# Optimization experiments

Measured on AMD Instinct MI355X. Metric: run time of the kernel, lower is better.

The kernel has to match this reference:

```python
import jax, jax.numpy as jnp
import numpy as np
from jax import lax

D, B, C, H, HD, FF, NC = 6, 32, 384, 6, 64, 1536, 10
IMG, P = 224, 16
N = (IMG // P) ** 2 + 1  # 197 tokens incl cls
SCALE = HD ** -0.5
EPS = 1e-6


def ln(x, w, b):
    m = jnp.mean(x, axis=-1, keepdims=True)
    v = jnp.var(x, axis=-1, keepdims=True)
    return (x - m) * lax.rsqrt(v + EPS) * w + b


def setup_inputs() -> dict:
    key = jax.random.key(0)
    ks = iter(jax.random.split(key, 40))
    rn = lambda shape, s=0.02: jax.random.normal(next(ks), shape, jnp.float32) * s
    inp = {
        'x': jax.random.normal(next(ks), (B, 3, IMG, IMG), jnp.float32),
        'y': jax.random.randint(next(ks), (B,), 0, NC),
        'patch_w': rn((C, 3, P, P)),
        'patch_b': rn((C,)),
        'cls_token': rn((1, 1, C)),
        'pos_embed': rn((1, N, C)),
        'n1_w': jnp.ones((D, C)), 'n1_b': jnp.zeros((D, C)),
        'qkv_w': rn((D, 3 * C, C)), 'qkv_b': rn((D, 3 * C)),
        'proj_w': rn((D, C, C)), 'proj_b': rn((D, C)),
        'mask_attn': jnp.ones((D, NC, H, HD)) + rn((D, NC, H, HD), 0.01),
        'mask_proj': jnp.ones((D, NC, C, C)) + rn((D, NC, C, C), 0.01),
        'n2_w': jnp.ones((D, C)), 'n2_b': jnp.zeros((D, C)),
        'fc1_w': rn((D, FF, C)), 'fc1_b': rn((D, FF)),
        'fc2_w': rn((D, C, FF)), 'fc2_b': rn((D, C)),
        'mask_fc1': jnp.ones((D, NC, FF, C)) + rn((D, NC, FF, C), 0.01),
        'mask_fc2': jnp.ones((D, NC, C, FF)) + rn((D, NC, C, FF), 0.01),
        'norm_w': jnp.ones((C,)), 'norm_b': jnp.zeros((C,)),
        'head_w': rn((NC, C)), 'head_b': jnp.zeros((NC,)),
    }
    return inp


def reference(x, y, patch_w, patch_b, cls_token, pos_embed, n1_w, n1_b, qkv_w,
              qkv_b, proj_w, proj_b, mask_attn, mask_proj, n2_w, n2_b,
              fc1_w, fc1_b, fc2_w, fc2_b, mask_fc1, mask_fc2,
              norm_w, norm_b, head_w, head_b):
    # patch embed: conv P x P stride P -> (B, C, 14, 14) -> (B, 196, C)
    h = lax.conv_general_dilated(x, patch_w, (P, P), 'VALID',
                                 dimension_numbers=('NCHW', 'OIHW', 'NCHW'))
    h = h.reshape(B, C, -1).transpose(0, 2, 1) + patch_b
    h = jnp.concatenate([jnp.broadcast_to(cls_token, (B, 1, C)), h], axis=1)
    h = h + pos_embed

    def block(xc, p):
        (w1n, b1n, qw, qb, pw, pb, ma, mp, w2n, b2n,
         f1w, f1b, f2w, f2b, mf1, mf2) = p
        t = ln(xc, w1n, b1n)
        qkv = (t @ qw.T + qb).reshape(B, N, 3, H, HD).transpose(2, 0, 3, 1, 4)
        q, k, v = qkv[0], qkv[1], qkv[2]  # (B,H,N,HD)
        a = jax.nn.softmax((q * SCALE) @ k.transpose(0, 1, 3, 2), axis=-1)
        o = a @ v  # (B,H,N,HD)
        o = o * ma[y][:, :, None, :]  # per-class head/dim mask
        o = o.transpose(0, 2, 1, 3).reshape(B, N, C)
        Wp = pw[None] * mp[y]  # (B,C,C) per-sample masked proj
        attn_out = jnp.einsum('bni,boi->bno', o, Wp) + pb
        xc = xc + attn_out
        t = ln(xc, w2n, b2n)
        W1 = f1w[None] * mf1[y]  # (B,FF,C)
        t = jnp.einsum('bni,boi->bno', t, W1) + f1b
        t = jax.nn.gelu(t, approximate=False)
        W2 = f2w[None] * mf2[y]  # (B,C,FF)
        t = jnp.einsum('bni,boi->bno', t, W2) + f2b
        return xc + t, None

    xs = (n1_w, n1_b, qkv_w, qkv_b, proj_w, proj_b, mask_attn, mask_proj,
          n2_w, n2_b, fc1_w, fc1_b, fc2_w, fc2_b, mask_fc1, mask_fc2)
    h, _ = lax.scan(block, h, xs)
    h = ln(h, norm_w, norm_b)
    cls = h[:, 0]  # (B, C)
    return cls @ head_w.T + head_b
```

## Files before the change

kernel.cpp:

```cpp
#include <hip/hip_runtime.h>
#include <hip/hip_bf16.h>
#include <math.h>

#define Dn 6
#define Bn 32
#define Cn 384
#define Hn 6
#define HDn 64
#define FFn 1536
#define NCn 10
#define IMGn 224
#define Nn 197
#define NPATCH 196
#define RP 256
#define TROWS 6400
#define SCALEf 0.125f
#define EPSf 1e-6f

typedef unsigned short u16;
typedef __attribute__((ext_vector_type(8))) short short8;
typedef __attribute__((ext_vector_type(4))) float f32x4;

__device__ __forceinline__ u16 f2bf(float f) {
    unsigned u = __float_as_uint(f);
    return (u16)((u + 0x7FFFu + ((u >> 16) & 1u)) >> 16);
}

__device__ __forceinline__ void gload16(const void* g, void* l) {
    __builtin_amdgcn_global_load_lds((const __attribute__((address_space(1))) void*)g,
                                     (__attribute__((address_space(3))) void*)l, 16, 0, 0);
}

__global__ __launch_bounds__(256) void cvtbf_kernel(const float* __restrict__ in,
                                                    u16* __restrict__ out) {
    long off = ((long)blockIdx.x * 256 + threadIdx.x) * 8;
    float4 v0 = *(const float4*)(in + off);
    float4 v1 = *(const float4*)(in + off + 4);
    short8 p;
    p[0] = f2bf(v0.x); p[1] = f2bf(v0.y); p[2] = f2bf(v0.z); p[3] = f2bf(v0.w);
    p[4] = f2bf(v1.x); p[5] = f2bf(v1.y); p[6] = f2bf(v1.z); p[7] = f2bf(v1.w);
    *(short8*)(out + off) = p;
}

__global__ __launch_bounds__(256) void maskmul3_kernel(
    const float* __restrict__ pw, const float* __restrict__ mp,
    const float* __restrict__ f1w, const float* __restrict__ mf1,
    const float* __restrict__ f2w, const float* __restrict__ mf2,
    u16* __restrict__ WMp, u16* __restrict__ WMf1, u16* __restrict__ WMf2) {
    const int seg = blockIdx.y;
    const unsigned bx = blockIdx.x;
    const float* W; const float* M; u16* O; int wi;
    if (seg == 0) {
        if (bx >= 720u) return;
        unsigned cls = bx / 72u;
        wi = (int)(bx - cls * 72u) * 2048 + threadIdx.x * 8;
        W = pw;
        M = mp + (long)cls * (Cn * Cn);
        O = WMp + (long)cls * (Cn * Cn);
    } else if (seg == 1) {
        unsigned cls = bx / 288u;
        wi = (int)(bx - cls * 288u) * 2048 + threadIdx.x * 8;
        W = f1w;
        M = mf1 + (long)cls * (FFn * Cn);
        O = WMf1 + (long)cls * (FFn * Cn);
    } else {
        unsigned cls = bx / 288u;
        wi = (int)(bx - cls * 288u) * 2048 + threadIdx.x * 8;
        W = f2w;
        M = mf2 + (long)cls * (Cn * FFn);
        O = WMf2 + (long)cls * (Cn * FFn);
    }
    float4 w0 = *(const float4*)(W + wi);
    float4 w1 = *(const float4*)(W + wi + 4);
    float4 m0 = *(const float4*)(M + wi);
    float4 m1 = *(const float4*)(M + wi + 4);
    short8 p;
    p[0] = f2bf(w0.x * m0.x); p[1] = f2bf(w0.y * m0.y);
    p[2] = f2bf(w0.z * m0.z); p[3] = f2bf(w0.w * m0.w);
    p[4] = f2bf(w1.x * m1.x); p[5] = f2bf(w1.y * m1.y);
    p[6] = f2bf(w1.z * m1.z); p[7] = f2bf(w1.w * m1.w);
    *(short8*)(O + wi) = p;
}

__global__ __launch_bounds__(256) void im2col_kernel(const float* __restrict__ x,
                                                     u16* __restrict__ col) {
    long idx = (long)blockIdx.x * 256 + threadIdx.x;
    int k = (int)(idx % 768);
    long row = idx / 768;
    int b = (int)(row / NPATCH), p = (int)(row % NPATCH);
    int i = k / 256, r = k % 256, ph = r / 16, pw = r % 16;
    int py = p / 14, px = p % 14;
    col[idx] = f2bf(x[(((long)b * 3 + i) * IMGn + py * 16 + ph) * IMGn + px * 16 + pw]);
}

__global__ __launch_bounds__(256) void assemble_kernel(const float* __restrict__ tmp,
                                                       const float* __restrict__ cls_token,
                                                       const float* __restrict__ pos,
                                                       float* __restrict__ x) {
    long idx = (long)blockIdx.x * 256 + threadIdx.x;
    int c = (int)(idx % Cn);
    long rem = idx / Cn;
    int n = (int)(rem % Nn);
    int b = (int)(rem / Nn);
    float v;
    if (n == 0) v = cls_token[c];
    else v = tmp[((long)b * NPATCH + (n - 1)) * Cn + c];
    x[((long)b * RP + n) * Cn + c] = v + pos[n * Cn + c];
}

__global__ __launch_bounds__(256) void pad_zero(float* __restrict__ X,
                                                u16* __restrict__ Tp) {
    int b = blockIdx.x;
    int tid = threadIdx.x;
    if (b == Bn) {
        u16* t0 = Tp + (long)Bn * Nn * Cn;
        for (int i = tid; i < (TROWS - Bn * Nn) * Cn; i += 256) t0[i] = 0;
        return;
    }
    float* Xb = X + ((long)b * RP + Nn) * Cn;
    for (int i = tid; i < (RP - Nn) * Cn; i += 256) Xb[i] = 0.f;
}

__global__ __launch_bounds__(64) void ln_kernel(const float* __restrict__ x,
                                                const float* __restrict__ w,
                                                const float* __restrict__ b,
                                                u16* __restrict__ out) {
    long blk = blockIdx.x;
    int bb = (int)(blk / Nn), n = (int)(blk % Nn);
    const float* xr = x + ((long)bb * RP + n) * Cn;
    u16* orow = out + ((long)bb * Nn + n) * Cn;
    int lane = threadIdx.x;
    float v[6];
    float s = 0.f, ss = 0.f;
#pragma unroll
    for (int j = 0; j < 6; ++j) {
        v[j] = xr[lane + 64 * j];
        s += v[j];
        ss += v[j] * v[j];
    }
#pragma unroll
    for (int off = 32; off >= 1; off >>= 1) {
        s += __shfl_xor(s, off);
        ss += __shfl_xor(ss, off);
    }
    float m = s * (1.0f / Cn);
    float var = ss * (1.0f / Cn) - m * m;
    float rstd = rsqrtf(var + EPSf);
#pragma unroll
    for (int j = 0; j < 6; ++j) {
        int c = lane + 64 * j;
        orow[c] = f2bf((v[j] - m) * rstd * w[c] + b[c]);
    }
}

template <int EPI, int MT>
__global__ __launch_bounds__(256) void gemm_bf16(
    const u16* __restrict__ A, long strideA,
    const u16* __restrict__ Wb, long wClassStride,
    const int* __restrict__ y,
    const float* __restrict__ bias,
    void* __restrict__ OutV, long strideO,
    int Nout, int Ktot) {
    const int bz = blockIdx.z;
    A += (long)bz * strideA;
    const u16* Wp = Wb + (y ? (long)y[bz] * wClassStride : 0);

    constexpr int ASUB = MT / 16;
    constexpr int AI = MT / 32;
    __shared__ alignas(16) u16 Ab[2][ASUB * 512];
    __shared__ alignas(16) u16 Bb[2][4096];

    const int tid = threadIdx.x;
    const int lane = tid & 63;
    const int w = tid >> 6;
    const int wr = w >> 1, wc = w & 1;
    const int m0 = blockIdx.x * MT;
    const int n0 = blockIdx.y * 128;
    const int r15 = lane & 15, oct = lane >> 4;

    auto STAGE = [&](int k0, int bf) {
        {
            int s0 = 2 * w;
            const u16* b0 = Wp + (long)(n0 + 16 * s0 + r15) * Ktot + k0 + oct * 8;
            gload16(b0, &Bb[bf][s0 * 512]);
            gload16(b0 + 16 * (long)Ktot, &Bb[bf][(s0 + 1) * 512]);
        }
        if (MT == 128) {
            int s0 = 2 * w;
            const u16* a0 = A + (long)(m0 + 16 * s0 + r15) * Ktot + k0 + oct * 8;
            gload16(a0, &Ab[bf][s0 * 512]);
            gload16(a0 + 16 * (long)Ktot, &Ab[bf][(s0 + 1) * 512]);
        } else {
            const u16* a0 = A + (long)(m0 + 16 * w + r15) * Ktot + k0 + oct * 8;
            gload16(a0, &Ab[bf][w * 512]);
        }
    };

    f32x4 acc[AI][4];
#pragma unroll
    for (int i = 0; i < AI; ++i)
#pragma unroll
        for (int j = 0; j < 4; ++j) acc[i][j] = (f32x4){0.f, 0.f, 0.f, 0.f};

    const int nsteps = Ktot / 32;
    STAGE(0, 0);
    __syncthreads();
    int cur = 0;
    for (int t = 0; t < nsteps; ++t) {
        if (t + 1 < nsteps) STAGE((t + 1) * 32, cur ^ 1);
        short8 af[AI], bfr[4];
#pragma unroll
        for (int i = 0; i < AI; ++i)
            af[i] = *(const short8*)(&Ab[cur][(wr * AI + i) * 512 + lane * 8]);
#pragma unroll
        for (int j = 0; j < 4; ++j)
            bfr[j] = *(const short8*)(&Bb[cur][(wc * 4 + j) * 512 + lane * 8]);
#pragma unroll
        for (int i = 0; i < AI; ++i)
#pragma unroll
            for (int j = 0; j < 4; ++j)
                acc[i][j] = __builtin_amdgcn_mfma_f32_16x16x32_bf16(af[i], bfr[j], acc[i][j], 0, 0, 0);
        __syncthreads();
        cur ^= 1;
    }

    const int lr = lane >> 4;
    const int lc = lane & 15;
#pragma unroll
    for (int i = 0; i < AI; ++i) {
#pragma unroll
        for (int j = 0; j < 4; ++j) {
            int colg = n0 + (wc * 4 + j) * 16 + lc;
            float bv = bias ? bias[colg] : 0.f;
#pragma unroll
            for (int r = 0; r < 4; ++r) {
                int m = m0 + (wr * AI + i) * 16 + lr * 4 + r;
                float v = acc[i][j][r] + bv;
                long oi = (long)m * Nout + colg;
                if (EPI == 0) {
                    ((u16*)OutV + (long)bz * strideO)[oi] = f2bf(v);
                } else if (EPI == 1) {
                    v = 0.5f * v * (1.0f + erff(v * 0.70710678118654752440f));
                    ((u16*)OutV + (long)bz * strideO)[oi] = f2bf(v);
                } else if (EPI == 2) {
                    ((float*)OutV + (long)bz * strideO)[oi] += v;
                } else {
                    ((float*)OutV + (long)bz * strideO)[oi] = v;
                }
            }
        }
    }
}

__global__ __launch_bounds__(256) void attn_fused(const u16* __restrict__ qkv,
                                                  const float* __restrict__ ma,
                                                  const int* __restrict__ y,
                                                  u16* __restrict__ O) {
    const int it = blockIdx.x;
    const int bh = blockIdx.y;
    const int h = bh % Hn, b = bh / Hn;
    const int i0 = it * 64;
    const int tid = threadIdx.x, lane = tid & 63, w = tid >> 6;
    const int lg = lane >> 4, lc = lane & 15;

    __shared__ alignas(16) u16 SH[31744];
    u16* Qb = SH;
    u16* Kb = SH + 4096;
    u16* Vb = SH;
    u16* Pb = SH + 17408;

    const u16* qkv_b = qkv + (long)b * Nn * (3 * Cn);
    const int r15 = lane & 15;
    const int oct = lane >> 4;

#pragma unroll
    for (int si = 0; si < 2; ++si) {
        int s = w * 2 + si;
        int r = (s >> 1) * 16 + r15;
        int g = (s & 1) * 4 + oct;
        const u16* src = qkv_b + (long)(i0 + r) * (3 * Cn) + h * HDn + g * 8;
        gload16(src, Qb + s * 512);
    }
    for (int s = w; s < 26; s += 4) {
        int c = (s >> 1) * 16 + r15;
        int g = (s & 1) * 4 + oct;
        const u16* src = qkv_b + (long)c * (3 * Cn) + Cn + h * HDn + g * 8;
        gload16(src, Kb + s * 512);
    }
    __syncthreads();

    f32x4 s[13];
#pragma unroll
    for (int jf = 0; jf < 13; ++jf) s[jf] = (f32x4){0.f, 0.f, 0.f, 0.f};
    {
        short8 a0 = *(const short8*)(Qb + (w * 2 + 0) * 512 + lane * 8);
        short8 a1 = *(const short8*)(Qb + (w * 2 + 1) * 512 + lane * 8);
#pragma unroll
        for (int jf = 0; jf < 13; ++jf) {
            short8 b0 = *(const short8*)(Kb + (jf * 2 + 0) * 512 + lane * 8);
            short8 b1 = *(const short8*)(Kb + (jf * 2 + 1) * 512 + lane * 8);
            s[jf] = __builtin_amdgcn_mfma_f32_16x16x32_bf16(a0, b0, s[jf], 0, 0, 0);
            s[jf] = __builtin_amdgcn_mfma_f32_16x16x32_bf16(a1, b1, s[jf], 0, 0, 0);
        }
    }

#pragma unroll
    for (int r = 0; r < 4; ++r) {
        float mx = -1e30f;
#pragma unroll
        for (int jf = 0; jf < 13; ++jf) {
            float v = s[jf][r] * SCALEf;
            if (jf * 16 + lc > 196) v = -1e30f;
            mx = fmaxf(mx, v);
        }
#pragma unroll
        for (int off = 1; off <= 8; off <<= 1) mx = fmaxf(mx, __shfl_xor(mx, off));
        float sum = 0.f;
#pragma unroll
        for (int jf = 0; jf < 13; ++jf) {
            float e = (jf * 16 + lc <= 196) ? __expf(s[jf][r] * SCALEf - mx) : 0.f;
            s[jf][r] = e;
            sum += e;
        }
#pragma unroll
        for (int off = 1; off <= 8; off <<= 1) sum += __shfl_xor(sum, off);
        float inv = 1.0f / sum;
#pragma unroll
        for (int jf = 0; jf < 13; ++jf) s[jf][r] *= inv;
    }
    __syncthreads();

    if (lane < 32) {
        short8 z = {0, 0, 0, 0, 0, 0, 0, 0};
        *(short8*)(Pb + (w * 7 + 6) * 512 + (32 + lane) * 8) = z;
    }
#pragma unroll
    for (int jf = 0; jf < 13; ++jf) {
#pragma unroll
        for (int r = 0; r < 4; ++r) {
            int col = jf * 16 + lc;
            int row = lg * 4 + r;
            Pb[(w * 7 + (col >> 5)) * 512 + (((col >> 3) & 3) * 16 + row) * 8 + (col & 7)] =
                (u16)f2bf(s[jf][r]);
        }
    }
    {
        const u16* vbase = qkv_b + 2 * Cn + h * HDn;
        const int jr = tid >> 3;
        const int d0 = (tid & 7) * 8;
        const int dsub = d0 >> 4;
        const int chi = d0 & 15;
        const int g = jr >> 3;
        const int e = jr & 7;
#pragma unroll
        for (int itv = 0; itv < 7; ++itv) {
            int j = jr + itv * 32;
            short8 v = *(const short8*)(vbase + (long)j * (3 * Cn) + d0);
            u16* dst = Vb + dsub * (7 * 512) + itv * 512 + (g * 16 + chi) * 8 + e;
#pragma unroll
            for (int t = 0; t < 8; ++t)
                dst[t * 8] = (u16)v[t];
        }
    }
    __syncthreads();

    f32x4 o[4];
#pragma unroll
    for (int df = 0; df < 4; ++df) o[df] = (f32x4){0.f, 0.f, 0.f, 0.f};
#pragma unroll
    for (int ks = 0; ks < 7; ++ks) {
        short8 pa = *(const short8*)(Pb + (w * 7 + ks) * 512 + lane * 8);
#pragma unroll
        for (int df = 0; df < 4; ++df) {
            short8 vb = *(const short8*)(Vb + (df * 7 + ks) * 512 + lane * 8);
            o[df] = __builtin_amdgcn_mfma_f32_16x16x32_bf16(pa, vb, o[df], 0, 0, 0);
        }
    }

    const float* mar = ma + (long)y[b] * (Hn * HDn) + h * HDn;
#pragma unroll
    for (int df = 0; df < 4; ++df) {
        int dcol = df * 16 + lc;
        float mk = mar[dcol];
#pragma unroll
        for (int r = 0; r < 4; ++r) {
            int i = i0 + w * 16 + lg * 4 + r;
            O[((long)b * RP + i) * Cn + h * HDn + dcol] = f2bf(o[df][r] * mk);
        }
    }
}

__global__ __launch_bounds__(64) void final_head(const float* __restrict__ x,
                                                 const float* __restrict__ nw,
                                                 const float* __restrict__ nb,
                                                 const float* __restrict__ hw,
                                                 const float* __restrict__ hb,
                                                 float* __restrict__ out) {
    int b = blockIdx.x;
    int lane = threadIdx.x;
    const float* xr = x + (long)b * RP * Cn;
    float v[6];
    float s = 0.f, ss = 0.f;
#pragma unroll
    for (int j = 0; j < 6; ++j) {
        v[j] = xr[lane + 64 * j];
        s += v[j];
        ss += v[j] * v[j];
    }
#pragma unroll
    for (int off = 32; off >= 1; off >>= 1) {
        s += __shfl_xor(s, off);
        ss += __shfl_xor(ss, off);
    }
    float m = s * (1.0f / Cn);
    float var = ss * (1.0f / Cn) - m * m;
    float rstd = rsqrtf(var + EPSf);
    float nvals[6];
#pragma unroll
    for (int j = 0; j < 6; ++j) {
        int c = lane + 64 * j;
        nvals[j] = (v[j] - m) * rstd * nw[c] + nb[c];
    }
    for (int c10 = 0; c10 < NCn; ++c10) {
        float p = 0.f;
#pragma unroll
        for (int j = 0; j < 6; ++j) p += nvals[j] * hw[(long)c10 * Cn + lane + 64 * j];
#pragma unroll
        for (int off = 32; off >= 1; off >>= 1) p += __shfl_xor(p, off);
        if (lane == 0) out[b * NCn + c10] = p + hb[c10];
    }
}

extern "C" void kernel_launch(void* const* d_in, const int* in_sizes, int n_in,
                              void* d_out, int out_size, void* d_ws, size_t ws_size,
                              hipStream_t stream) {
    const float* x_in     = (const float*)d_in[0];
    const int*   y        = (const int*)d_in[1];
    const float* patch_w  = (const float*)d_in[2];
    const float* patch_b  = (const float*)d_in[3];
    const float* cls_tok  = (const float*)d_in[4];
    const float* pos_emb  = (const float*)d_in[5];
    const float* n1_w     = (const float*)d_in[6];
    const float* n1_b     = (const float*)d_in[7];
    const float* qkv_w    = (const float*)d_in[8];
    const float* qkv_b    = (const float*)d_in[9];
    const float* proj_w   = (const float*)d_in[10];
    const float* proj_b   = (const float*)d_in[11];
    const float* mask_attn= (const float*)d_in[12];
    const float* mask_proj= (const float*)d_in[13];
    const float* n2_w     = (const float*)d_in[14];
    const float* n2_b     = (const float*)d_in[15];
    const float* fc1_w    = (const float*)d_in[16];
    const float* fc1_b    = (const float*)d_in[17];
    const float* fc2_w    = (const float*)d_in[18];
    const float* fc2_b    = (const float*)d_in[19];
    const float* mask_fc1 = (const float*)d_in[20];
    const float* mask_fc2 = (const float*)d_in[21];
    const float* norm_w   = (const float*)d_in[22];
    const float* norm_b   = (const float*)d_in[23];
    const float* head_w   = (const float*)d_in[24];
    const float* head_b   = (const float*)d_in[25];

    char* base = (char*)d_ws;
    float* X    = (float*)base;   base += (long)Bn * RP * Cn * 4;
    u16*   Tp   = (u16*)base;     base += (long)TROWS * Cn * 2;
    u16*   QKV  = (u16*)base;     base += (long)TROWS * 3 * Cn * 2;
    u16*   O    = (u16*)base;     base += (long)Bn * RP * Cn * 2;
    u16*   FFb  = (u16*)base;     base += (long)Bn * RP * FFn * 2;
    u16*   COL  = (u16*)base;     base += (long)Bn * NPATCH * 768 * 2;
    u16*   WQ   = (u16*)base;     base += (long)Dn * 3 * Cn * Cn * 2;
    u16*   WP   = (u16*)base;     base += (long)Cn * 768 * 2;
    u16*   WMp  = (u16*)base;     base += (long)Dn * NCn * Cn * Cn * 2;
    u16*   WMf1 = (u16*)base;     base += (long)Dn * NCn * FFn * Cn * 2;
    u16*   WMf2 = (u16*)base;     base += (long)Dn * NCn * Cn * FFn * 2;
    float* PTMP = (float*)FFb;

    const long sX = (long)RP * Cn;
    const long sTp = (long)Nn * Cn;
    const long sF = (long)RP * FFn;

    cvtbf_kernel<<<1296, 256, 0, stream>>>(qkv_w, WQ);
    cvtbf_kernel<<<144, 256, 0, stream>>>(patch_w, WP);
    for (int l = 0; l < Dn; ++l) {
        maskmul3_kernel<<<dim3(2880, 3), 256, 0, stream>>>(
            proj_w + (long)l * Cn * Cn, mask_proj + (long)l * NCn * Cn * Cn,
            fc1_w + (long)l * FFn * Cn, mask_fc1 + (long)l * NCn * FFn * Cn,
            fc2_w + (long)l * Cn * FFn, mask_fc2 + (long)l * NCn * Cn * FFn,
            WMp + (long)l * NCn * Cn * Cn,
            WMf1 + (long)l * NCn * FFn * Cn,
            WMf2 + (long)l * NCn * Cn * FFn);
    }

    im2col_kernel<<<18816, 256, 0, stream>>>(x_in, COL);
    gemm_bf16<3, 64><<<dim3(98, 3, 1), 256, 0, stream>>>(
        COL, 0, WP, 0, nullptr, patch_b, PTMP, 0, Cn, 768);
    assemble_kernel<<<9456, 256, 0, stream>>>(PTMP, cls_tok, pos_emb, X);
    pad_zero<<<Bn + 1, 256, 0, stream>>>(X, Tp);
    ln_kernel<<<Bn * Nn, 64, 0, stream>>>(X, n1_w, n1_b, Tp);

    for (int l = 0; l < Dn; ++l) {
        const u16* WMp_l  = WMp  + (long)l * NCn * Cn * Cn;
        const u16* WMf1_l = WMf1 + (long)l * NCn * FFn * Cn;
        const u16* WMf2_l = WMf2 + (long)l * NCn * Cn * FFn;

        gemm_bf16<0, 64><<<dim3(100, 9, 1), 256, 0, stream>>>(
            Tp, 0, WQ + (long)l * 3 * Cn * Cn, 0, nullptr, qkv_b + (long)l * 3 * Cn,
            QKV, 0, 3 * Cn, Cn);
        attn_fused<<<dim3(4, Bn * Hn), 256, 0, stream>>>(
            QKV, mask_attn + (long)l * NCn * Hn * HDn, y, O);
        gemm_bf16<2, 64><<<dim3(4, 3, Bn), 256, 0, stream>>>(
            O, sX, WMp_l, (long)Cn * Cn, y, proj_b + l * Cn, X, sX, Cn, Cn);
        ln_kernel<<<Bn * Nn, 64, 0, stream>>>(X, n2_w + l * Cn, n2_b + l * Cn, Tp);
        gemm_bf16<1, 128><<<dim3(2, 12, Bn), 256, 0, stream>>>(
            Tp, sTp, WMf1_l, (long)FFn * Cn, y, fc1_b + (long)l * FFn, FFb, sF, FFn, Cn);
        gemm_bf16<2, 64><<<dim3(4, 3, Bn), 256, 0, stream>>>(
            FFb, sF, WMf2_l, (long)Cn * FFn, y, fc2_b + l * Cn, X, sX, Cn, FFn);
        if (l + 1 < Dn)
            ln_kernel<<<Bn * Nn, 64, 0, stream>>>(X, n1_w + (l + 1) * Cn, n1_b + (l + 1) * Cn, Tp);
    }

    final_head<<<Bn, 64, 0, stream>>>(X, norm_w, norm_b, head_w, head_b, (float*)d_out);
}
```

Baseline: 1.087 ms.

## Merge per-layer maskmul launches, rework V transpose load, enlarge QKV GEMM tile

The six per-layer mask-multiply launches become one launch with a layer grid dimension, which removes launch overhead and tail gaps. The V staging in attention now has each thread gather eight strided scalars and write one 16-byte LDS store, replacing sixteen-byte global loads followed by scattered scalar LDS writes. The QKV GEMM switches to a 128-row tile with half as many blocks. The V gather loses global load coalescing in exchange for fewer LDS stores, and the larger QKV tile lowers block count and may hurt occupancy.

```diff
diff --git a/kernel.cpp b/kernel.cpp
--- a/kernel.cpp
+++ b/kernel.cpp
@@ -42,11 +42,12 @@
     *(short8*)(out + off) = p;
 }
 
-__global__ __launch_bounds__(256) void maskmul3_kernel(
+__global__ __launch_bounds__(256) void maskmul_all(
     const float* __restrict__ pw, const float* __restrict__ mp,
     const float* __restrict__ f1w, const float* __restrict__ mf1,
     const float* __restrict__ f2w, const float* __restrict__ mf2,
     u16* __restrict__ WMp, u16* __restrict__ WMf1, u16* __restrict__ WMf2) {
+    const int l = blockIdx.z;
     const int seg = blockIdx.y;
     const unsigned bx = blockIdx.x;
     const float* W; const float* M; u16* O; int wi;
@@ -54,21 +55,21 @@
         if (bx >= 720u) return;
         unsigned cls = bx / 72u;
         wi = (int)(bx - cls * 72u) * 2048 + threadIdx.x * 8;
-        W = pw;
-        M = mp + (long)cls * (Cn * Cn);
-        O = WMp + (long)cls * (Cn * Cn);
+        W = pw + (long)l * (Cn * Cn);
+        M = mp + ((long)l * NCn + cls) * (Cn * Cn);
+        O = WMp + ((long)l * NCn + cls) * (Cn * Cn);
     } else if (seg == 1) {
         unsigned cls = bx / 288u;
         wi = (int)(bx - cls * 288u) * 2048 + threadIdx.x * 8;
-        W = f1w;
-        M = mf1 + (long)cls * (FFn * Cn);
-        O = WMf1 + (long)cls * (FFn * Cn);
+        W = f1w + (long)l * (FFn * Cn);
+        M = mf1 + ((long)l * NCn + cls) * (FFn * Cn);
+        O = WMf1 + ((long)l * NCn + cls) * (FFn * Cn);
     } else {
         unsigned cls = bx / 288u;
         wi = (int)(bx - cls * 288u) * 2048 + threadIdx.x * 8;
-        W = f2w;
-        M = mf2 + (long)cls * (Cn * FFn);
-        O = WMf2 + (long)cls * (Cn * FFn);
+        W = f2w + (long)l * (Cn * FFn);
+        M = mf2 + ((long)l * NCn + cls) * (Cn * FFn);
+        O = WMf2 + ((long)l * NCn + cls) * (Cn * FFn);
     }
     float4 w0 = *(const float4*)(W + wi);
     float4 w1 = *(const float4*)(W + wi + 4);
@@ -345,21 +346,17 @@
         }
     }
     {
-        const u16* vbase = qkv_b + 2 * Cn + h * HDn;
-        const int jr = tid >> 3;
-        const int d0 = (tid & 7) * 8;
-        const int dsub = d0 >> 4;
-        const int chi = d0 & 15;
-        const int g = jr >> 3;
-        const int e = jr & 7;
-#pragma unroll
-        for (int itv = 0; itv < 7; ++itv) {
-            int j = jr + itv * 32;
-            short8 v = *(const short8*)(vbase + (long)j * (3 * Cn) + d0);
-            u16* dst = Vb + dsub * (7 * 512) + itv * 512 + (g * 16 + chi) * 8 + e;
+        const u16* vbase = qkv_b + 2 * Cn + h * HDn + (tid & 63);
+        int d = tid & 63;
+#pragma unroll
+        for (int k = 0; k < 7; ++k) {
+            int jo = (tid >> 6) + 4 * k;
+            short8 p;
 #pragma unroll
             for (int t = 0; t < 8; ++t)
-                dst[t * 8] = (u16)v[t];
+                p[t] = (short)vbase[(long)(jo * 8 + t) * (3 * Cn)];
+            *(short8*)(Vb + (d >> 4) * (7 * 512) + (jo >> 2) * 512 +
+                       ((jo & 3) * 16 + (d & 15)) * 8) = p;
         }
     }
     __syncthreads();
@@ -481,15 +478,8 @@
 
     cvtbf_kernel<<<1296, 256, 0, stream>>>(qkv_w, WQ);
     cvtbf_kernel<<<144, 256, 0, stream>>>(patch_w, WP);
-    for (int l = 0; l < Dn; ++l) {
-        maskmul3_kernel<<<dim3(2880, 3), 256, 0, stream>>>(
-            proj_w + (long)l * Cn * Cn, mask_proj + (long)l * NCn * Cn * Cn,
-            fc1_w + (long)l * FFn * Cn, mask_fc1 + (long)l * NCn * FFn * Cn,
-            fc2_w + (long)l * Cn * FFn, mask_fc2 + (long)l * NCn * Cn * FFn,
-            WMp + (long)l * NCn * Cn * Cn,
-            WMf1 + (long)l * NCn * FFn * Cn,
-            WMf2 + (long)l * NCn * Cn * FFn);
-    }
+    maskmul_all<<<dim3(2880, 3, Dn), 256, 0, stream>>>(
+        proj_w, mask_proj, fc1_w, mask_fc1, fc2_w, mask_fc2, WMp, WMf1, WMf2);
 
     im2col_kernel<<<18816, 256, 0, stream>>>(x_in, COL);
     gemm_bf16<3, 64><<<dim3(98, 3, 1), 256, 0, stream>>>(
@@ -503,7 +493,7 @@
         const u16* WMf1_l = WMf1 + (long)l * NCn * FFn * Cn;
         const u16* WMf2_l = WMf2 + (long)l * NCn * Cn * FFn;
 
-        gemm_bf16<0, 64><<<dim3(100, 9, 1), 256, 0, stream>>>(
+        gemm_bf16<0, 128><<<dim3(50, 9, 1), 256, 0, stream>>>(
             Tp, 0, WQ + (long)l * 3 * Cn * Cn, 0, nullptr, qkv_b + (long)l * 3 * Cn,
             QKV, 0, 3 * Cn, Cn);
         attn_fused<<<dim3(4, Bn * Hn), 256, 0, stream>>>(
```

Result: faster. 1.053 ms (-3.1%).
